# Kernel optimization log

Hardware: AMD Instinct MI355X
Metric: run time of the kernel (lower is better)

The kernel has to match this reference:

```python
import jax, jax.numpy as jnp
import numpy as np

# RoIAlign config (matches init_kwargs)
OUT_H = OUT_W = 7
SPATIAL_SCALE = 0.25
SAMPLING_RATIO = 2  # fixed grid per bin (aligned=True, detectron2-style)
N_IMG, C, H, W = 2, 256, 200, 304
N_ROIS = 512


def setup_inputs() -> dict:
    key = jax.random.key(0)
    kf, kb, kx1, ky1, kw, kh = jax.random.split(key, 6)
    features = jax.random.normal(kf, (N_IMG, C, H, W), dtype=jnp.float32)
    # rois: [R,5] = (batch_idx, x1, y1, x2, y2) in input-image coords (image ~ 1216x800)
    bidx = jax.random.randint(kb, (N_ROIS,), 0, N_IMG).astype(jnp.float32)
    x1 = jax.random.uniform(kx1, (N_ROIS,), minval=0.0, maxval=1100.0)
    y1 = jax.random.uniform(ky1, (N_ROIS,), minval=0.0, maxval=700.0)
    bw = jax.random.uniform(kw, (N_ROIS,), minval=8.0, maxval=116.0)
    bh = jax.random.uniform(kh, (N_ROIS,), minval=8.0, maxval=100.0)
    rois = jnp.stack([bidx, x1, y1, x1 + bw, y1 + bh], axis=1).astype(jnp.float32)
    return {"features": features, "rois": rois}


def roi_align(features, rois):
    N, C_, H_, W_ = features.shape
    G = SAMPLING_RATIO
    b = rois[:, 0].astype(jnp.int32)
    # aligned=True: scale then shift by -0.5 (continuous pixel model)
    x1 = rois[:, 1] * SPATIAL_SCALE - 0.5
    y1 = rois[:, 2] * SPATIAL_SCALE - 0.5
    x2 = rois[:, 3] * SPATIAL_SCALE - 0.5
    y2 = rois[:, 4] * SPATIAL_SCALE - 0.5
    roi_w = x2 - x1  # aligned: no clamp to min 1
    roi_h = y2 - y1
    bin_w = roi_w / OUT_W
    bin_h = roi_h / OUT_H

    # sample coordinates: per roi, OUT*G points along each axis
    iy = jnp.arange(OUT_H * G)
    ix = jnp.arange(OUT_W * G)
    # y = y1 + ph*bin_h + (s+0.5)*bin_h/G
    ys = y1[:, None] + (iy // G) * bin_h[:, None] + ((iy % G) + 0.5) * bin_h[:, None] / G  # [R, OUT_H*G]
    xs = x1[:, None] + (ix // G) * bin_w[:, None] + ((ix % G) + 0.5) * bin_w[:, None] / G  # [R, OUT_W*G]

    y = ys[:, :, None]  # [R, Py, 1]
    x = xs[:, None, :]  # [R, 1, Px]
    valid = ((y > -1.0) & (y < H_) & (x > -1.0) & (x < W_)).astype(features.dtype)  # [R,Py,Px]

    yc = jnp.clip(y, 0.0, H_ - 1)
    xc = jnp.clip(x, 0.0, W_ - 1)
    y0 = jnp.floor(yc).astype(jnp.int32)
    x0 = jnp.floor(xc).astype(jnp.int32)
    y1i = jnp.minimum(y0 + 1, H_ - 1)
    x1i = jnp.minimum(x0 + 1, W_ - 1)
    ly = yc - y0
    lx = xc - x0
    hy = 1.0 - ly
    hx = 1.0 - lx

    badv = b[:, None, None]
    Py, Px = OUT_H * G, OUT_W * G
    y0b = jnp.broadcast_to(y0, (rois.shape[0], Py, Px))
    y1b = jnp.broadcast_to(y1i, (rois.shape[0], Py, Px))
    x0b = jnp.broadcast_to(x0, (rois.shape[0], Py, Px))
    x1b = jnp.broadcast_to(x1i, (rois.shape[0], Py, Px))

    # advanced indexing: [R,Py,Px,C]
    v00 = features[badv, :, y0b, x0b]
    v01 = features[badv, :, y0b, x1b]
    v10 = features[badv, :, y1b, x0b]
    v11 = features[badv, :, y1b, x1b]

    w00 = (hy * hx) * valid
    w01 = (hy * lx) * valid
    w10 = (ly * hx) * valid
    w11 = (ly * lx) * valid

    samp = (w00[..., None] * v00 + w01[..., None] * v01 +
            w10[..., None] * v10 + w11[..., None] * v11)  # [R,Py,Px,C]
    # average pool over the GxG samples per bin
    R = rois.shape[0]
    out = samp.reshape(R, OUT_H, G, OUT_W, G, C_).mean(axis=(2, 4))  # [R,OUT_H,OUT_W,C]
    return jnp.transpose(out, (0, 3, 1, 2))  # [R,C,OUT_H,OUT_W]


def reference(features, rois):
    return roi_align(features, rois)
```

## Files before the change

kernel.cpp:

```cpp
#include <hip/hip_runtime.h>


#define OUT_H 7
#define OUT_W 7
constexpr float SPATIAL_SCALE = 0.25f;
constexpr int CN = 256;
constexpr int FH = 200;
constexpr int FW = 304;
constexpr int N_IMG = 2;
constexpr int N_ROIS = 512;
constexpr size_t PLANE = (size_t)FH * FW;
constexpr size_t NHWC_ELEMS = (size_t)N_IMG * PLANE * CN;
constexpr size_t NHWC_BF16_BYTES = NHWC_ELEMS * sizeof(unsigned short);

__device__ __forceinline__ unsigned short f2bf_rne(float f) {
    unsigned int u = __float_as_uint(f);
    unsigned int r = (u + 0x7FFFu + ((u >> 16) & 1u)) >> 16;
    return (unsigned short)r;
}

__global__ __launch_bounds__(256) void nchw_to_nhwc_bf16(
    const float* __restrict__ in, unsigned short* __restrict__ ws)
{
    const int nh = blockIdx.x;
    const int n = nh / FH;
    const int h = nh % FH;
    const int c = threadIdx.x;
    const int w0 = blockIdx.y * 16;

    const float* src = in + (((size_t)n * CN + c) * FH + h) * FW + w0;
    unsigned short* dst = ws + (((size_t)n * FH + h) * FW + w0) * CN + c;

    float4 v0 = *(const float4*)(src + 0);
    float4 v1 = *(const float4*)(src + 4);
    float4 v2 = *(const float4*)(src + 8);
    float4 v3 = *(const float4*)(src + 12);

    const float vals[16] = {v0.x, v0.y, v0.z, v0.w, v1.x, v1.y, v1.z, v1.w,
                            v2.x, v2.y, v2.z, v2.w, v3.x, v3.y, v3.z, v3.w};
#pragma unroll
    for (int i = 0; i < 16; ++i) {
        dst[(size_t)i * CN] = f2bf_rne(vals[i]);
    }
}

__global__ __launch_bounds__(128) void roi_align_roi_block(
    const unsigned short* __restrict__ ws,
    const float* __restrict__ rois,
    float* __restrict__ out)
{
    const int r = blockIdx.x;
    const int t = threadIdx.x;

    __shared__ float s_roi[5];
    __shared__ int   s_off[196][4];
    __shared__ float s_w[196][4];
    __shared__ int   s_b;

    if (t < 5) s_roi[t] = rois[r * 5 + t];
    __syncthreads();

    const float x1 = s_roi[1] * SPATIAL_SCALE - 0.5f;
    const float y1 = s_roi[2] * SPATIAL_SCALE - 0.5f;
    const float x2 = s_roi[3] * SPATIAL_SCALE - 0.5f;
    const float y2 = s_roi[4] * SPATIAL_SCALE - 0.5f;
    const float bin_w = (x2 - x1) / OUT_W;
    const float bin_h = (y2 - y1) / OUT_H;

    for (int s = t; s < 196; s += 128) {
        const int iy = s / 14;
        const int ix = s % 14;
        const float y = y1 + (iy >> 1) * bin_h + ((iy & 1) + 0.5f) * bin_h * 0.5f;
        const float x = x1 + (ix >> 1) * bin_w + ((ix & 1) + 0.5f) * bin_w * 0.5f;
        const float validf =
            (y > -1.0f && y < (float)FH && x > -1.0f && x < (float)FW) ? 1.0f : 0.0f;
        const float yc = fminf(fmaxf(y, 0.0f), (float)(FH - 1));
        const float xc = fminf(fmaxf(x, 0.0f), (float)(FW - 1));
        const int y0 = (int)floorf(yc);
        const int x0 = (int)floorf(xc);
        const int y1i = min(y0 + 1, FH - 1);
        const int x1i = min(x0 + 1, FW - 1);
        const float ly = yc - (float)y0;
        const float lx = xc - (float)x0;
        const float hy = 1.0f - ly;
        const float hx = 1.0f - lx;
        s_off[s][0] = (y0  * FW + x0 ) * CN;
        s_off[s][1] = (y0  * FW + x1i) * CN;
        s_off[s][2] = (y1i * FW + x0 ) * CN;
        s_off[s][3] = (y1i * FW + x1i) * CN;
        s_w[s][0] = hy * hx * validf;
        s_w[s][1] = hy * lx * validf;
        s_w[s][2] = ly * hx * validf;
        s_w[s][3] = ly * lx * validf;
    }
    if (t == 0) s_b = (int)s_roi[0];
    __syncthreads();

    const unsigned short* base = ws + (size_t)s_b * (PLANE * CN) + 2 * t;
    const size_t outbase = ((size_t)r * CN + 2 * t) * (OUT_H * OUT_W);

#pragma unroll 1
    for (int ph = 0; ph < OUT_H; ++ph) {
        float acc0[OUT_W] = {0.f, 0.f, 0.f, 0.f, 0.f, 0.f, 0.f};
        float acc1[OUT_W] = {0.f, 0.f, 0.f, 0.f, 0.f, 0.f, 0.f};
#pragma unroll
        for (int gy = 0; gy < 2; ++gy) {
            const int iy = 2 * ph + gy;
#pragma unroll
            for (int ix = 0; ix < 14; ++ix) {
                const int s = iy * 14 + ix;
                const int pw = ix >> 1;
#pragma unroll
                for (int k = 0; k < 4; ++k) {
                    const unsigned int u = *(const unsigned int*)(base + s_off[s][k]);
                    const float f0 = __uint_as_float(u << 16);
                    const float f1 = __uint_as_float(u & 0xFFFF0000u);
                    const float w = s_w[s][k];
                    acc0[pw] = fmaf(w, f0, acc0[pw]);
                    acc1[pw] = fmaf(w, f1, acc1[pw]);
                }
            }
        }
        const size_t ob = outbase + (size_t)ph * OUT_W;
#pragma unroll
        for (int pw = 0; pw < OUT_W; ++pw) {
            out[ob + pw] = acc0[pw] * 0.25f;
            out[ob + (OUT_H * OUT_W) + pw] = acc1[pw] * 0.25f;
        }
    }
}

__global__ __launch_bounds__(256) void roi_align_nchw(
    const float* __restrict__ feat,
    const float* __restrict__ rois,
    float* __restrict__ out)
{
    const int r  = blockIdx.x;
    const int ph = blockIdx.y;
    const int c  = threadIdx.x;

    __shared__ float s_roi[5];
    __shared__ int   s_off[28][4];
    __shared__ float s_w[28][4];
    __shared__ int   s_b;

    if (threadIdx.x < 5) s_roi[threadIdx.x] = rois[r * 5 + threadIdx.x];
    __syncthreads();

    if (threadIdx.x < 28) {
        const int s  = threadIdx.x;
        const int gy = s / 14;
        const int ix = s % 14;
        const float x1 = s_roi[1] * SPATIAL_SCALE - 0.5f;
        const float y1 = s_roi[2] * SPATIAL_SCALE - 0.5f;
        const float x2 = s_roi[3] * SPATIAL_SCALE - 0.5f;
        const float y2 = s_roi[4] * SPATIAL_SCALE - 0.5f;
        const float bin_w = (x2 - x1) / OUT_W;
        const float bin_h = (y2 - y1) / OUT_H;
        const float y = y1 + ph * bin_h + (gy + 0.5f) * bin_h * 0.5f;
        const int px = ix >> 1;
        const int gx = ix & 1;
        const float x = x1 + px * bin_w + (gx + 0.5f) * bin_w * 0.5f;
        const float validf =
            (y > -1.0f && y < (float)FH && x > -1.0f && x < (float)FW) ? 1.0f : 0.0f;
        const float yc = fminf(fmaxf(y, 0.0f), (float)(FH - 1));
        const float xc = fminf(fmaxf(x, 0.0f), (float)(FW - 1));
        const int y0 = (int)floorf(yc);
        const int x0 = (int)floorf(xc);
        const int y1i = min(y0 + 1, FH - 1);
        const int x1i = min(x0 + 1, FW - 1);
        const float ly = yc - (float)y0;
        const float lx = xc - (float)x0;
        const float hy = 1.0f - ly;
        const float hx = 1.0f - lx;
        s_off[s][0] = y0  * FW + x0;
        s_off[s][1] = y0  * FW + x1i;
        s_off[s][2] = y1i * FW + x0;
        s_off[s][3] = y1i * FW + x1i;
        s_w[s][0] = hy * hx * validf;
        s_w[s][1] = hy * lx * validf;
        s_w[s][2] = ly * hx * validf;
        s_w[s][3] = ly * lx * validf;
    }
    if (threadIdx.x == 0) s_b = (int)s_roi[0];
    __syncthreads();

    const float* base = feat + ((size_t)s_b * CN + c) * PLANE;

    float acc[OUT_W] = {0.f, 0.f, 0.f, 0.f, 0.f, 0.f, 0.f};
#pragma unroll
    for (int s = 0; s < 28; ++s) {
        const float v0 = base[s_off[s][0]];
        const float v1 = base[s_off[s][1]];
        const float v2 = base[s_off[s][2]];
        const float v3 = base[s_off[s][3]];
        acc[(s % 14) >> 1] += s_w[s][0] * v0 + s_w[s][1] * v1 +
                              s_w[s][2] * v2 + s_w[s][3] * v3;
    }

    const size_t outbase = ((size_t)r * CN + c) * (OUT_H * OUT_W) + (size_t)ph * OUT_W;
#pragma unroll
    for (int pw = 0; pw < OUT_W; ++pw) {
        out[outbase + pw] = acc[pw] * 0.25f;
    }
}

extern "C" void kernel_launch(void* const* d_in, const int* in_sizes, int n_in,
                              void* d_out, int out_size, void* d_ws, size_t ws_size,
                              hipStream_t stream) {
    const float* feat = (const float*)d_in[0];
    const float* rois = (const float*)d_in[1];
    float* out = (float*)d_out;

    if (ws_size >= NHWC_BF16_BYTES) {
        unsigned short* ws = (unsigned short*)d_ws;
        dim3 tgrid(N_IMG * FH, FW / 16, 1);
        nchw_to_nhwc_bf16<<<tgrid, dim3(256, 1, 1), 0, stream>>>(feat, ws);
        roi_align_roi_block<<<dim3(N_ROIS, 1, 1), dim3(128, 1, 1), 0, stream>>>(ws, rois, out);
    } else {
        dim3 grid(N_ROIS, OUT_H, 1);
        roi_align_nchw<<<grid, dim3(256, 1, 1), 0, stream>>>(feat, rois, out);
    }
}
```

Before: 246.8 us.

## Split RoI align across output rows and pack bf16 pairs in transpose

The transpose kernel now has each thread handle two channels, packing two bf16 values into one 32-bit store instead of issuing 16-bit scattered stores. The RoI align kernel now launches one block per (roi, output row) instead of one block per roi. This gives 7x more blocks and lets each thread keep all 28 samples of a row in flight. Block indices are swizzled so that 8 consecutive blocks cover different rois for the same row. The cost is repeated per-block setup and roi loads.

After: 229.3 us. -7.1%, faster.

```diff
diff --git a/kernel.cpp b/kernel.cpp
--- a/kernel.cpp
+++ b/kernel.cpp
@@ -19,63 +19,77 @@
     return (unsigned short)r;
 }
 
-__global__ __launch_bounds__(256) void nchw_to_nhwc_bf16(
+__global__ __launch_bounds__(128) void nchw_to_nhwc_bf16(
     const float* __restrict__ in, unsigned short* __restrict__ ws)
 {
     const int nh = blockIdx.x;
     const int n = nh / FH;
     const int h = nh % FH;
-    const int c = threadIdx.x;
+    const int c0 = 2 * threadIdx.x;
     const int w0 = blockIdx.y * 16;
 
-    const float* src = in + (((size_t)n * CN + c) * FH + h) * FW + w0;
-    unsigned short* dst = ws + (((size_t)n * FH + h) * FW + w0) * CN + c;
-
-    float4 v0 = *(const float4*)(src + 0);
-    float4 v1 = *(const float4*)(src + 4);
-    float4 v2 = *(const float4*)(src + 8);
-    float4 v3 = *(const float4*)(src + 12);
-
-    const float vals[16] = {v0.x, v0.y, v0.z, v0.w, v1.x, v1.y, v1.z, v1.w,
-                            v2.x, v2.y, v2.z, v2.w, v3.x, v3.y, v3.z, v3.w};
+    const float* src0 = in + (((size_t)n * CN + c0) * FH + h) * FW + w0;
+    const float* src1 = src0 + (size_t)FH * FW;
+    unsigned int* dst =
+        (unsigned int*)(ws + (((size_t)n * FH + h) * FW + w0) * CN + c0);
+
+    float4 a0 = *(const float4*)(src0 + 0);
+    float4 a1 = *(const float4*)(src0 + 4);
+    float4 a2 = *(const float4*)(src0 + 8);
+    float4 a3 = *(const float4*)(src0 + 12);
+    float4 b0 = *(const float4*)(src1 + 0);
+    float4 b1 = *(const float4*)(src1 + 4);
+    float4 b2 = *(const float4*)(src1 + 8);
+    float4 b3 = *(const float4*)(src1 + 12);
+
+    const float va[16] = {a0.x, a0.y, a0.z, a0.w, a1.x, a1.y, a1.z, a1.w,
+                          a2.x, a2.y, a2.z, a2.w, a3.x, a3.y, a3.z, a3.w};
+    const float vb[16] = {b0.x, b0.y, b0.z, b0.w, b1.x, b1.y, b1.z, b1.w,
+                          b2.x, b2.y, b2.z, b2.w, b3.x, b3.y, b3.z, b3.w};
 #pragma unroll
     for (int i = 0; i < 16; ++i) {
-        dst[(size_t)i * CN] = f2bf_rne(vals[i]);
-    }
-}
-
-__global__ __launch_bounds__(128) void roi_align_roi_block(
+        const unsigned int lo = f2bf_rne(va[i]);
+        const unsigned int hi = f2bf_rne(vb[i]);
+        dst[(size_t)i * (CN / 2)] = lo | (hi << 16);
+    }
+}
+
+__global__ __launch_bounds__(128) void roi_align_nhwc_bf16(
     const unsigned short* __restrict__ ws,
     const float* __restrict__ rois,
     float* __restrict__ out)
 {
-    const int r = blockIdx.x;
-    const int t = threadIdx.x;
+    const int b = blockIdx.x;
+    const int x = b & 7;
+    const int s_id = b >> 3;
+    const int r  = (s_id / 7) * 8 + x;
+    const int ph = s_id % 7;
+    const int t  = threadIdx.x;
 
     __shared__ float s_roi[5];
-    __shared__ int   s_off[196][4];
-    __shared__ float s_w[196][4];
+    __shared__ int   s_off[28][4];
+    __shared__ float s_w[28][4];
     __shared__ int   s_b;
 
     if (t < 5) s_roi[t] = rois[r * 5 + t];
     __syncthreads();
 
-    const float x1 = s_roi[1] * SPATIAL_SCALE - 0.5f;
-    const float y1 = s_roi[2] * SPATIAL_SCALE - 0.5f;
-    const float x2 = s_roi[3] * SPATIAL_SCALE - 0.5f;
-    const float y2 = s_roi[4] * SPATIAL_SCALE - 0.5f;
-    const float bin_w = (x2 - x1) / OUT_W;
-    const float bin_h = (y2 - y1) / OUT_H;
-
-    for (int s = t; s < 196; s += 128) {
-        const int iy = s / 14;
+    if (t < 28) {
+        const int s  = t;
+        const int gy = s / 14;
         const int ix = s % 14;
-        const float y = y1 + (iy >> 1) * bin_h + ((iy & 1) + 0.5f) * bin_h * 0.5f;
-        const float x = x1 + (ix >> 1) * bin_w + ((ix & 1) + 0.5f) * bin_w * 0.5f;
+        const float x1 = s_roi[1] * SPATIAL_SCALE - 0.5f;
+        const float y1 = s_roi[2] * SPATIAL_SCALE - 0.5f;
+        const float x2 = s_roi[3] * SPATIAL_SCALE - 0.5f;
+        const float y2 = s_roi[4] * SPATIAL_SCALE - 0.5f;
+        const float bin_w = (x2 - x1) / OUT_W;
+        const float bin_h = (y2 - y1) / OUT_H;
+        const float y = y1 + ph * bin_h + (gy + 0.5f) * bin_h * 0.5f;
+        const float xf = x1 + (ix >> 1) * bin_w + ((ix & 1) + 0.5f) * bin_w * 0.5f;
         const float validf =
-            (y > -1.0f && y < (float)FH && x > -1.0f && x < (float)FW) ? 1.0f : 0.0f;
+            (y > -1.0f && y < (float)FH && xf > -1.0f && xf < (float)FW) ? 1.0f : 0.0f;
         const float yc = fminf(fmaxf(y, 0.0f), (float)(FH - 1));
-        const float xc = fminf(fmaxf(x, 0.0f), (float)(FW - 1));
+        const float xc = fminf(fmaxf(xf, 0.0f), (float)(FW - 1));
         const int y0 = (int)floorf(yc);
         const int x0 = (int)floorf(xc);
         const int y1i = min(y0 + 1, FH - 1);
@@ -97,36 +111,28 @@
     __syncthreads();
 
     const unsigned short* base = ws + (size_t)s_b * (PLANE * CN) + 2 * t;
-    const size_t outbase = ((size_t)r * CN + 2 * t) * (OUT_H * OUT_W);
-
-#pragma unroll 1
-    for (int ph = 0; ph < OUT_H; ++ph) {
-        float acc0[OUT_W] = {0.f, 0.f, 0.f, 0.f, 0.f, 0.f, 0.f};
-        float acc1[OUT_W] = {0.f, 0.f, 0.f, 0.f, 0.f, 0.f, 0.f};
-#pragma unroll
-        for (int gy = 0; gy < 2; ++gy) {
-            const int iy = 2 * ph + gy;
-#pragma unroll
-            for (int ix = 0; ix < 14; ++ix) {
-                const int s = iy * 14 + ix;
-                const int pw = ix >> 1;
-#pragma unroll
-                for (int k = 0; k < 4; ++k) {
-                    const unsigned int u = *(const unsigned int*)(base + s_off[s][k]);
-                    const float f0 = __uint_as_float(u << 16);
-                    const float f1 = __uint_as_float(u & 0xFFFF0000u);
-                    const float w = s_w[s][k];
-                    acc0[pw] = fmaf(w, f0, acc0[pw]);
-                    acc1[pw] = fmaf(w, f1, acc1[pw]);
-                }
-            }
+
+    float acc0[OUT_W] = {0.f, 0.f, 0.f, 0.f, 0.f, 0.f, 0.f};
+    float acc1[OUT_W] = {0.f, 0.f, 0.f, 0.f, 0.f, 0.f, 0.f};
+#pragma unroll
+    for (int s = 0; s < 28; ++s) {
+        const int pw = (s % 14) >> 1;
+#pragma unroll
+        for (int k = 0; k < 4; ++k) {
+            const unsigned int u = *(const unsigned int*)(base + s_off[s][k]);
+            const float f0 = __uint_as_float(u << 16);
+            const float f1 = __uint_as_float(u & 0xFFFF0000u);
+            const float w = s_w[s][k];
+            acc0[pw] = fmaf(w, f0, acc0[pw]);
+            acc1[pw] = fmaf(w, f1, acc1[pw]);
         }
-        const size_t ob = outbase + (size_t)ph * OUT_W;
-#pragma unroll
-        for (int pw = 0; pw < OUT_W; ++pw) {
-            out[ob + pw] = acc0[pw] * 0.25f;
-            out[ob + (OUT_H * OUT_W) + pw] = acc1[pw] * 0.25f;
-        }
+    }
+
+    const size_t outbase = ((size_t)r * CN + 2 * t) * (OUT_H * OUT_W) + (size_t)ph * OUT_W;
+#pragma unroll
+    for (int pw = 0; pw < OUT_W; ++pw) {
+        out[outbase + pw] = acc0[pw] * 0.25f;
+        out[outbase + (OUT_H * OUT_W) + pw] = acc1[pw] * 0.25f;
     }
 }
 
@@ -158,13 +164,11 @@
         const float bin_w = (x2 - x1) / OUT_W;
         const float bin_h = (y2 - y1) / OUT_H;
         const float y = y1 + ph * bin_h + (gy + 0.5f) * bin_h * 0.5f;
-        const int px = ix >> 1;
-        const int gx = ix & 1;
-        const float x = x1 + px * bin_w + (gx + 0.5f) * bin_w * 0.5f;
+        const float xf = x1 + (ix >> 1) * bin_w + ((ix & 1) + 0.5f) * bin_w * 0.5f;
         const float validf =
-            (y > -1.0f && y < (float)FH && x > -1.0f && x < (float)FW) ? 1.0f : 0.0f;
+            (y > -1.0f && y < (float)FH && xf > -1.0f && xf < (float)FW) ? 1.0f : 0.0f;
         const float yc = fminf(fmaxf(y, 0.0f), (float)(FH - 1));
-        const float xc = fminf(fmaxf(x, 0.0f), (float)(FW - 1));
+        const float xc = fminf(fmaxf(xf, 0.0f), (float)(FW - 1));
         const int y0 = (int)floorf(yc);
         const int x0 = (int)floorf(xc);
         const int y1i = min(y0 + 1, FH - 1);
@@ -215,8 +219,9 @@
     if (ws_size >= NHWC_BF16_BYTES) {
         unsigned short* ws = (unsigned short*)d_ws;
         dim3 tgrid(N_IMG * FH, FW / 16, 1);
-        nchw_to_nhwc_bf16<<<tgrid, dim3(256, 1, 1), 0, stream>>>(feat, ws);
-        roi_align_roi_block<<<dim3(N_ROIS, 1, 1), dim3(128, 1, 1), 0, stream>>>(ws, rois, out);
+        nchw_to_nhwc_bf16<<<tgrid, dim3(128, 1, 1), 0, stream>>>(feat, ws);
+        roi_align_nhwc_bf16<<<dim3(N_ROIS * OUT_H, 1, 1), dim3(128, 1, 1), 0, stream>>>(
+            ws, rois, out);
     } else {
         dim3 grid(N_ROIS, OUT_H, 1);
         roi_align_nchw<<<grid, dim3(256, 1, 1), 0, stream>>>(feat, rois, out);
```
